# Kernel optimization log

Hardware: AMD Instinct MI355X
Metric: run time of the kernel (lower is better)

## Reference

```python
import jax, jax.numpy as jnp
import numpy as np

NUM_HEADS = 16


def setup_inputs() -> dict:
    key = jax.random.key(0)
    ks = jax.random.split(key, 6)
    B, S, D = 2, 2048, 1024
    x = jax.random.normal(ks[0], (B, S, D), dtype=jnp.float32)
    # Linear weights stored as [d_in, d_out] so forward is x @ W (qkv_bias=False)
    scale = 1.0 / np.sqrt(D)
    Wq = jax.random.normal(ks[1], (D, D), dtype=jnp.float32) * scale
    Wk = jax.random.normal(ks[2], (D, D), dtype=jnp.float32) * scale
    Wv = jax.random.normal(ks[3], (D, D), dtype=jnp.float32) * scale
    Wo = jax.random.normal(ks[4], (D, D), dtype=jnp.float32) * scale
    bo = jax.random.normal(ks[5], (D,), dtype=jnp.float32) * 0.01
    return {"x": x, "Wq": Wq, "Wk": Wk, "Wv": Wv, "Wo": Wo, "bo": bo}


def reference(x, Wq, Wk, Wv, Wo, bo):
    B, S, D = x.shape
    H = NUM_HEADS
    hd = D // H

    def split_heads(t):  # [B,S,D] -> [B,H,S,hd]
        return t.reshape(B, S, H, hd).transpose(0, 2, 1, 3)

    q = split_heads(x @ Wq)
    k = split_heads(x @ Wk)
    v = split_heads(x @ Wv)

    # full score matrix [B,H,S,S]
    scores = jnp.einsum('bhsd,bhtd->bhst', q, k)
    causal = jnp.triu(jnp.ones((S, S), dtype=bool), k=1)
    scores = jnp.where(causal, -jnp.inf, scores)
    attn = jax.nn.softmax(scores * (hd ** -0.5), axis=-1)
    # dropout p=0.0 -> identity
    out = jnp.einsum('bhst,bhtd->bhsd', attn, v)
    out = out.transpose(0, 2, 1, 3).reshape(B, S, D)
    return out @ Wo + bo
```

## Files before the change

kernel.cpp:

```cpp
#include <hip/hip_runtime.h>

typedef unsigned short ushort_t;
typedef unsigned int uint_t;
typedef __attribute__((ext_vector_type(8))) short short8;
typedef __attribute__((ext_vector_type(4))) float floatx4;

#define S_LEN 2048
#define D_DIM 1024
#define H_NUM 16
#define HD 64
#define GBUF (128 * 32)

__device__ __forceinline__ float bf2f(ushort_t u) {
    union { uint_t i; float f; } c; c.i = ((uint_t)u) << 16; return c.f;
}
__device__ __forceinline__ ushort_t f2bf(float f) {
    union { float f; uint_t i; } c; c.f = f;
    uint_t r = c.i + 0x7fffu + ((c.i >> 16) & 1u);
    return (ushort_t)(r >> 16);
}

__device__ __forceinline__ void g2l16(const ushort_t* g, ushort_t* l) {
    __builtin_amdgcn_global_load_lds(
        (const __attribute__((address_space(1))) void*)g,
        (__attribute__((address_space(3))) void*)l, 16, 0, 0);
}

__global__ __launch_bounds__(256, 4) void cast_x_kernel(
        const float* __restrict__ in, ushort_t* __restrict__ out) {
    const int idx = (blockIdx.x * 256 + threadIdx.x) * 4;
    const float4 v = *(const float4*)(in + idx);
    ushort4 o;
    o.x = f2bf(v.x); o.y = f2bf(v.y); o.z = f2bf(v.z); o.w = f2bf(v.w);
    *(ushort4*)(out + idx) = o;
}

__global__ __launch_bounds__(256, 2) void transpose4_kernel(
        const float* __restrict__ W0, const float* __restrict__ W1,
        const float* __restrict__ W2, const float* __restrict__ W3,
        ushort_t* __restrict__ T0, ushort_t* __restrict__ T1,
        ushort_t* __restrict__ T2, ushort_t* __restrict__ T3) {
    const int z = blockIdx.z;
    const float* in  = (z == 0) ? W0 : (z == 1) ? W1 : (z == 2) ? W2 : W3;
    ushort_t*    out = (z == 0) ? T0 : (z == 1) ? T1 : (z == 2) ? T2 : T3;
    __shared__ __align__(16) ushort_t t[64][65];
    const int r0 = blockIdx.y * 64, c0 = blockIdx.x * 64;
    const int tr = threadIdx.x >> 4;
    const int tc = (threadIdx.x & 15) * 4;
#pragma unroll
    for (int i = 0; i < 4; ++i) {
        const int row = tr + i * 16;
        const float4 v = *(const float4*)(in + (size_t)(r0 + row) * D_DIM + c0 + tc);
        t[row][tc + 0] = f2bf(v.x); t[row][tc + 1] = f2bf(v.y);
        t[row][tc + 2] = f2bf(v.z); t[row][tc + 3] = f2bf(v.w);
    }
    __syncthreads();
#pragma unroll
    for (int i = 0; i < 4; ++i) {
        const int n = tr + i * 16;
        ushort4 v;
        v.x = t[tc + 0][n]; v.y = t[tc + 1][n];
        v.z = t[tc + 2][n]; v.w = t[tc + 3][n];
        *(ushort4*)(out + (size_t)(c0 + n) * D_DIM + r0 + tc) = v;
    }
}

__device__ __forceinline__ void gemm_tile(
        const ushort_t* __restrict__ A, const ushort_t* __restrict__ BT,
        const int m0, const int n0,
        ushort_t* As, ushort_t* Bs, floatx4 acc[4][4]) {
    const int tid  = threadIdx.x;
    const int w    = tid >> 6;
    const int wm   = (w >> 1) * 64;
    const int wn   = (w & 1) * 64;
    const int lrow = tid & 15;
    const int kq   = ((tid & 63) >> 4) * 8;

    const int flat0 = tid * 8;
    const int flat1 = (256 + tid) * 8;
    const int row0 = flat0 >> 5, kk0 = flat0 & 31;
    const int row1 = flat1 >> 5, kk1 = flat1 & 31;

    const ushort_t* ga0 = A  + (size_t)(m0 + row0) * D_DIM + kk0;
    const ushort_t* gb0 = BT + (size_t)(n0 + row0) * D_DIM + kk0;
    const ushort_t* ga1 = A  + (size_t)(m0 + row1) * D_DIM + kk1;
    const ushort_t* gb1 = BT + (size_t)(n0 + row1) * D_DIM + kk1;

    const int nsteps = D_DIM / 32;

    g2l16(ga0, As + flat0);
    g2l16(gb0, Bs + flat0);
    g2l16(ga1, As + flat1);
    g2l16(gb1, Bs + flat1);
    g2l16(ga0 + 32, As + GBUF + flat0);
    g2l16(gb0 + 32, Bs + GBUF + flat0);
    g2l16(ga1 + 32, As + GBUF + flat1);
    g2l16(gb1 + 32, Bs + GBUF + flat1);

    int cur = 0;
    for (int k = 0; k < nsteps; ++k) {
        if (k == nsteps - 1)
            asm volatile("s_waitcnt vmcnt(0) lgkmcnt(0)" ::: "memory");
        else
            asm volatile("s_waitcnt vmcnt(4) lgkmcnt(0)" ::: "memory");
        __builtin_amdgcn_sched_barrier(0);
        __builtin_amdgcn_s_barrier();

        const ushort_t* Ac = As + cur * GBUF;
        const ushort_t* Bc = Bs + cur * GBUF;
        short8 av[4], bv[4];
#pragma unroll
        for (int i = 0; i < 4; ++i)
            av[i] = *(const short8*)(Ac + (wm + i * 16 + lrow) * 32 + kq);
#pragma unroll
        for (int j = 0; j < 4; ++j)
            bv[j] = *(const short8*)(Bc + (wn + j * 16 + lrow) * 32 + kq);

        if (k + 2 < nsteps) {
            const int nb = (cur + 2 >= 3) ? cur - 1 : cur + 2;
            ushort_t* An = As + nb * GBUF;
            ushort_t* Bn = Bs + nb * GBUF;
            const int ko = (k + 2) * 32;
            g2l16(ga0 + ko, An + flat0);
            g2l16(gb0 + ko, Bn + flat0);
            g2l16(ga1 + ko, An + flat1);
            g2l16(gb1 + ko, Bn + flat1);
        }

#pragma unroll
        for (int i = 0; i < 4; ++i)
#pragma unroll
            for (int j = 0; j < 4; ++j)
                acc[i][j] = __builtin_amdgcn_mfma_f32_16x16x32_bf16(
                    av[i], bv[j], acc[i][j], 0, 0, 0);

        cur = (cur + 1 >= 3) ? 0 : cur + 1;
    }
}

__global__ __launch_bounds__(256, 3) void gemm_qkv_kernel(
        const ushort_t* __restrict__ A,
        const ushort_t* __restrict__ WqT, const ushort_t* __restrict__ WkT,
        const ushort_t* __restrict__ WvT,
        ushort_t* __restrict__ Qo, ushort_t* __restrict__ Ko,
        ushort_t* __restrict__ Vo) {
    const ushort_t* BT = (blockIdx.z == 0) ? WqT : (blockIdx.z == 1) ? WkT : WvT;
    ushort_t* C        = (blockIdx.z == 0) ? Qo  : (blockIdx.z == 1) ? Ko  : Vo;
    const float sc     = (blockIdx.z == 0) ? 0.18033688f : 1.0f;
    __shared__ __align__(16) ushort_t As[3 * GBUF];
    __shared__ __align__(16) ushort_t Bs[3 * GBUF];
    const int m0 = blockIdx.y * 128, n0 = blockIdx.x * 128;

    floatx4 acc[4][4] = {};
    gemm_tile(A, BT, m0, n0, As, Bs, acc);

    const int tid = threadIdx.x;
    const int w = tid >> 6, wm = (w >> 1) * 64, wn = (w & 1) * 64;
    const int lrow = tid & 15;
    const int rquad = ((tid & 63) >> 4) * 4;
#pragma unroll
    for (int i = 0; i < 4; ++i) {
        const int mbase = m0 + wm + i * 16 + rquad;
#pragma unroll
        for (int j = 0; j < 4; ++j) {
            const int gn = n0 + wn + j * 16 + lrow;
#pragma unroll
            for (int r = 0; r < 4; ++r)
                C[(size_t)(mbase + r) * D_DIM + gn] = f2bf(acc[i][j][r] * sc);
        }
    }
}

__global__ __launch_bounds__(256, 2) void gemm_out_kernel(
        const ushort_t* __restrict__ A, const ushort_t* __restrict__ WoT,
        const float* __restrict__ bias, float* __restrict__ C) {
    __shared__ __align__(16) ushort_t As[3 * GBUF];
    __shared__ __align__(16) ushort_t Bs[3 * GBUF];
    const int m0 = blockIdx.y * 128, n0 = blockIdx.x * 128;

    floatx4 acc[4][4] = {};
    gemm_tile(A, WoT, m0, n0, As, Bs, acc);

    const int tid = threadIdx.x;
    const int w = tid >> 6, wm = (w >> 1) * 64, wn = (w & 1) * 64;
    const int lrow = tid & 15;
    const int rquad = ((tid & 63) >> 4) * 4;
#pragma unroll
    for (int i = 0; i < 4; ++i) {
        const int mbase = m0 + wm + i * 16 + rquad;
#pragma unroll
        for (int j = 0; j < 4; ++j) {
            const int gn = n0 + wn + j * 16 + lrow;
            const float badd = bias[gn];
#pragma unroll
            for (int r = 0; r < 4; ++r)
                C[(size_t)(mbase + r) * D_DIM + gn] = acc[i][j][r] + badd;
        }
    }
}

__global__ __launch_bounds__(256, 4) void attn_mfma_kernel(
        const ushort_t* __restrict__ Q, const ushort_t* __restrict__ K,
        const ushort_t* __restrict__ V, ushort_t* __restrict__ O) {
    __shared__ __align__(16) ushort_t Ks[64 * 64];
    __shared__ __align__(16) ushort_t Vt[64 * 64];
    __shared__ __align__(16) ushort_t Ps[4][16 * 64];

    const int bh  = blockIdx.x;
    const int b   = bh >> 4, h = bh & 15;
    const int g   = blockIdx.y & 7;
    const int p   = blockIdx.y >> 3;
    const int qt  = (p == 0) ? g : (p == 1) ? (15 - g)
                  : (p == 2) ? (16 + g) : (31 - g);
    const int q0  = qt * 64;
    const int tid = threadIdx.x;
    const int wq  = tid >> 6;
    const int lane = tid & 63;
    const int col  = lane & 15;
    const int quad = lane >> 4;
    const int c7 = col & 7;
    const int qw0  = q0 + wq * 16;
    const size_t rowbase = (size_t)b * S_LEN;
    const int ch0 = h * HD;

    const int skey = tid >> 2;
    const int schk = tid & 3;
    const int vkp = tid & 31;
    const int vdc = tid >> 5;

    short8 aq[2];
#pragma unroll
    for (int kc = 0; kc < 2; ++kc)
        aq[kc] = *(const short8*)(Q + (rowbase + qw0 + col) * D_DIM
                                    + ch0 + kc * 32 + quad * 8);

    floatx4 oacc[4] = {};
    float mrun[4], lrun[4];
#pragma unroll
    for (int r = 0; r < 4; ++r) { mrun[r] = -1e30f; lrun[r] = 0.0f; }

    const int ntiles = qt + 1;

    short8 krA, krB, vrA, vrB;
    {
        const ushort_t* kg = K + (rowbase + skey) * D_DIM + ch0 + schk * 16;
        krA = *(const short8*)(kg);
        krB = *(const short8*)(kg + 8);
        const ushort_t* vg = V + (rowbase + 2 * vkp) * D_DIM + ch0 + vdc * 8;
        vrA = *(const short8*)(vg);
        vrB = *(const short8*)(vg + D_DIM);
    }

    for (int t = 0; t < ntiles; ++t) {
        const int kb = t * 64;
        __syncthreads();
        {
            const int sw = skey & 7;
            *(short8*)(Ks + skey * 64 + (((2 * schk) ^ sw) << 3)) = krA;
            *(short8*)(Ks + skey * 64 + (((2 * schk + 1) ^ sw) << 3)) = krB;
        }
#pragma unroll
        for (int e = 0; e < 8; ++e) {
            const int d = vdc * 8 + e;
            const uint_t pk = (uint_t)(ushort_t)vrA[e] | ((uint_t)(ushort_t)vrB[e] << 16);
            *(uint_t*)(Vt + d * 64 + ((2 * vkp) ^ ((d & 7) << 3))) = pk;
        }
        {
            const int kbn = (t + 1 < ntiles) ? (t + 1) * 64 : 0;
            const ushort_t* kg = K + (rowbase + kbn + skey) * D_DIM + ch0 + schk * 16;
            krA = *(const short8*)(kg);
            krB = *(const short8*)(kg + 8);
            const ushort_t* vg = V + (rowbase + kbn + 2 * vkp) * D_DIM + ch0 + vdc * 8;
            vrA = *(const short8*)(vg);
            vrB = *(const short8*)(vg + D_DIM);
        }
        __syncthreads();

        if (kb <= qw0 + 15) {
            floatx4 sa[4] = {};
            __builtin_amdgcn_s_setprio(1);
#pragma unroll
            for (int kc = 0; kc < 2; ++kc)
#pragma unroll
                for (int j = 0; j < 4; ++j) {
                    const short8 bk = *(const short8*)(
                        Ks + (j * 16 + col) * 64 + (((kc * 4 + quad) ^ c7) << 3));
                    sa[j] = __builtin_amdgcn_mfma_f32_16x16x32_bf16(
                        aq[kc], bk, sa[j], 0, 0, 0);
                }
            __builtin_amdgcn_s_setprio(0);

            const bool needmask = (kb + 63 > qw0);
            if (needmask) {
#pragma unroll
                for (int j = 0; j < 4; ++j)
#pragma unroll
                    for (int r = 0; r < 4; ++r) {
                        const int row = qw0 + quad * 4 + r;
                        const int key = kb + j * 16 + col;
                        if (key > row) sa[j][r] = -1e30f;
                    }
            }
#pragma unroll
            for (int r = 0; r < 4; ++r) {
                float mx = fmaxf(fmaxf(sa[0][r], sa[1][r]),
                                 fmaxf(sa[2][r], sa[3][r]));
                mx = fmaxf(mx, __shfl_xor(mx, 1));
                mx = fmaxf(mx, __shfl_xor(mx, 2));
                mx = fmaxf(mx, __shfl_xor(mx, 4));
                mx = fmaxf(mx, __shfl_xor(mx, 8));
                const float mn = fmaxf(mrun[r], mx);
                const float al = __builtin_amdgcn_exp2f(mrun[r] - mn);
                mrun[r] = mn;
                float rs = 0.0f;
#pragma unroll
                for (int j = 0; j < 4; ++j) {
                    const float p2 = __builtin_amdgcn_exp2f(sa[j][r] - mn);
                    sa[j][r] = p2;
                    rs += p2;
                }
                lrun[r] = lrun[r] * al + rs;
#pragma unroll
                for (int jd = 0; jd < 4; ++jd) oacc[jd][r] *= al;
            }
            {
                ushort_t* pw = Ps[wq];
#pragma unroll
                for (int j = 0; j < 4; ++j)
#pragma unroll
                    for (int r = 0; r < 4; ++r) {
                        const int row = quad * 4 + r;
                        pw[row * 64 + ((j * 16 + col) ^ ((row & 7) << 3))] =
                            f2bf(sa[j][r]);
                    }
            }
            asm volatile("s_waitcnt lgkmcnt(0)" ::: "memory");
            __builtin_amdgcn_s_setprio(1);
#pragma unroll
            for (int kc = 0; kc < 2; ++kc) {
                const short8 ap = *(const short8*)(
                    Ps[wq] + col * 64 + (((kc * 4 + quad) ^ c7) << 3));
#pragma unroll
                for (int jd = 0; jd < 4; ++jd) {
                    const short8 bv = *(const short8*)(
                        Vt + (jd * 16 + col) * 64 + (((kc * 4 + quad) ^ c7) << 3));
                    oacc[jd] = __builtin_amdgcn_mfma_f32_16x16x32_bf16(
                        ap, bv, oacc[jd], 0, 0, 0);
                }
            }
            __builtin_amdgcn_s_setprio(0);
        }
    }

#pragma unroll
    for (int r = 0; r < 4; ++r) {
        float l = lrun[r];
        l += __shfl_xor(l, 1);
        l += __shfl_xor(l, 2);
        l += __shfl_xor(l, 4);
        l += __shfl_xor(l, 8);
        const int row = qw0 + quad * 4 + r;
        const float inv = 1.0f / l;
#pragma unroll
        for (int jd = 0; jd < 4; ++jd)
            O[(rowbase + row) * D_DIM + ch0 + jd * 16 + col] =
                f2bf(oacc[jd][r] * inv);
    }
}

extern "C" void kernel_launch(void* const* d_in, const int* in_sizes, int n_in,
                              void* d_out, int out_size, void* d_ws, size_t ws_size,
                              hipStream_t stream) {
    const float* x  = (const float*)d_in[0];
    const float* Wq = (const float*)d_in[1];
    const float* Wk = (const float*)d_in[2];
    const float* Wv = (const float*)d_in[3];
    const float* Wo = (const float*)d_in[4];
    const float* bo = (const float*)d_in[5];
    float* out = (float*)d_out;

    char* ws = (char*)d_ws;
    const size_t MB = 1024 * 1024;
    ushort_t* xb  = (ushort_t*)(ws + 0 * MB);
    ushort_t* WqT = (ushort_t*)(ws + 8 * MB);
    ushort_t* WkT = (ushort_t*)(ws + 10 * MB);
    ushort_t* WvT = (ushort_t*)(ws + 12 * MB);
    ushort_t* WoT = (ushort_t*)(ws + 14 * MB);
    ushort_t* Qb  = (ushort_t*)(ws + 16 * MB);
    ushort_t* Kb  = (ushort_t*)(ws + 24 * MB);
    ushort_t* Vb  = (ushort_t*)(ws + 32 * MB);
    ushort_t* Ob  = (ushort_t*)(ws + 40 * MB);

    cast_x_kernel<<<4096, 256, 0, stream>>>(x, xb);
    transpose4_kernel<<<dim3(16, 16, 4), 256, 0, stream>>>(
        Wq, Wk, Wv, Wo, WqT, WkT, WvT, WoT);

    gemm_qkv_kernel<<<dim3(8, 32, 3), 256, 0, stream>>>(
        xb, WqT, WkT, WvT, Qb, Kb, Vb);

    attn_mfma_kernel<<<dim3(32, 32), 256, 0, stream>>>(Qb, Kb, Vb, Ob);

    gemm_out_kernel<<<dim3(8, 32), 256, 0, stream>>>(Ob, WoT, bo, out);
}
```

Measured before the change: 194.8 us.

## Compute S transposed and pass P to PV MFMA via register permutes

Swaps the MFMA operands so each lane holds scores for one query row, which turns the row max and sum into two cross-lane shuffles instead of four per row. The probabilities are packed with the hardware bf16 convert and rearranged into the A-operand layout with ds_bpermute, so the per-wave shared-memory P buffer and its wait are gone. The rescale factors and final normalizer are broadcast back to the output layout with bpermute. This trades LDS stores and loads for more permute instructions and extra register pressure.

```diff
diff --git a/kernel.cpp b/kernel.cpp
--- a/kernel.cpp
+++ b/kernel.cpp
@@ -18,6 +18,11 @@
     union { float f; uint_t i; } c; c.f = f;
     uint_t r = c.i + 0x7fffu + ((c.i >> 16) & 1u);
     return (ushort_t)(r >> 16);
+}
+__device__ __forceinline__ uint_t cvtpk_bf16(float lo, float hi) {
+    uint_t d;
+    asm("v_cvt_pk_bf16_f32 %0, %1, %2" : "=v"(d) : "v"(lo), "v"(hi));
+    return d;
 }
 
 __device__ __forceinline__ void g2l16(const ushort_t* g, ushort_t* l) {
@@ -204,7 +209,6 @@
         const ushort_t* __restrict__ V, ushort_t* __restrict__ O) {
     __shared__ __align__(16) ushort_t Ks[64 * 64];
     __shared__ __align__(16) ushort_t Vt[64 * 64];
-    __shared__ __align__(16) ushort_t Ps[4][16 * 64];
 
     const int bh  = blockIdx.x;
     const int b   = bh >> 4, h = bh & 15;
@@ -222,6 +226,8 @@
     const int qw0  = q0 + wq * 16;
     const size_t rowbase = (size_t)b * S_LEN;
     const int ch0 = h * HD;
+    const int q4 = quad * 4;
+    const int gbase = (lane & 48) << 2;
 
     const int skey = tid >> 2;
     const int schk = tid & 3;
@@ -235,9 +241,7 @@
                                     + ch0 + kc * 32 + quad * 8);
 
     floatx4 oacc[4] = {};
-    float mrun[4], lrun[4];
-#pragma unroll
-    for (int r = 0; r < 4; ++r) { mrun[r] = -1e30f; lrun[r] = 0.0f; }
+    float mrun0 = -1e30f, lrun0 = 0.0f;
 
     const int ntiles = qt + 1;
 
@@ -262,8 +266,8 @@
 #pragma unroll
         for (int e = 0; e < 8; ++e) {
             const int d = vdc * 8 + e;
-            const uint_t pk = (uint_t)(ushort_t)vrA[e] | ((uint_t)(ushort_t)vrB[e] << 16);
-            *(uint_t*)(Vt + d * 64 + ((2 * vkp) ^ ((d & 7) << 3))) = pk;
+            const uint_t pkv = (uint_t)(ushort_t)vrA[e] | ((uint_t)(ushort_t)vrB[e] << 16);
+            *(uint_t*)(Vt + d * 64 + ((2 * vkp) ^ ((d & 7) << 3))) = pkv;
         }
         {
             const int kbn = (t + 1 < ntiles) ? (t + 1) * 64 : 0;
@@ -286,81 +290,95 @@
                     const short8 bk = *(const short8*)(
                         Ks + (j * 16 + col) * 64 + (((kc * 4 + quad) ^ c7) << 3));
                     sa[j] = __builtin_amdgcn_mfma_f32_16x16x32_bf16(
-                        aq[kc], bk, sa[j], 0, 0, 0);
+                        bk, aq[kc], sa[j], 0, 0, 0);
                 }
             __builtin_amdgcn_s_setprio(0);
 
             const bool needmask = (kb + 63 > qw0);
             if (needmask) {
+                const int qrow = qw0 + col;
 #pragma unroll
                 for (int j = 0; j < 4; ++j)
 #pragma unroll
-                    for (int r = 0; r < 4; ++r) {
-                        const int row = qw0 + quad * 4 + r;
-                        const int key = kb + j * 16 + col;
-                        if (key > row) sa[j][r] = -1e30f;
-                    }
+                    for (int r = 0; r < 4; ++r)
+                        if (kb + j * 16 + q4 + r > qrow) sa[j][r] = -1e30f;
             }
-#pragma unroll
-            for (int r = 0; r < 4; ++r) {
-                float mx = fmaxf(fmaxf(sa[0][r], sa[1][r]),
-                                 fmaxf(sa[2][r], sa[3][r]));
-                mx = fmaxf(mx, __shfl_xor(mx, 1));
-                mx = fmaxf(mx, __shfl_xor(mx, 2));
-                mx = fmaxf(mx, __shfl_xor(mx, 4));
-                mx = fmaxf(mx, __shfl_xor(mx, 8));
-                const float mn = fmaxf(mrun[r], mx);
-                const float al = __builtin_amdgcn_exp2f(mrun[r] - mn);
-                mrun[r] = mn;
-                float rs = 0.0f;
-#pragma unroll
-                for (int j = 0; j < 4; ++j) {
+            float mx = sa[0][0];
+#pragma unroll
+            for (int j = 0; j < 4; ++j)
+#pragma unroll
+                for (int r = 0; r < 4; ++r) mx = fmaxf(mx, sa[j][r]);
+            mx = fmaxf(mx, __shfl_xor(mx, 16));
+            mx = fmaxf(mx, __shfl_xor(mx, 32));
+            const float mn = fmaxf(mrun0, mx);
+            const float al = __builtin_amdgcn_exp2f(mrun0 - mn);
+            mrun0 = mn;
+            float rs = 0.0f;
+#pragma unroll
+            for (int j = 0; j < 4; ++j)
+#pragma unroll
+                for (int r = 0; r < 4; ++r) {
                     const float p2 = __builtin_amdgcn_exp2f(sa[j][r] - mn);
                     sa[j][r] = p2;
                     rs += p2;
                 }
-                lrun[r] = lrun[r] * al + rs;
-#pragma unroll
-                for (int jd = 0; jd < 4; ++jd) oacc[jd][r] *= al;
+            lrun0 = lrun0 * al + rs;
+            float al4[4];
+#pragma unroll
+            for (int r = 0; r < 4; ++r)
+                al4[r] = __int_as_float(__builtin_amdgcn_ds_bpermute(
+                    gbase + ((q4 + r) << 2), __float_as_int(al)));
+#pragma unroll
+            for (int jd = 0; jd < 4; ++jd)
+#pragma unroll
+                for (int r = 0; r < 4; ++r) oacc[jd][r] *= al4[r];
+            uint_t pk[4][2];
+#pragma unroll
+            for (int j = 0; j < 4; ++j) {
+                pk[j][0] = cvtpk_bf16(sa[j][0], sa[j][1]);
+                pk[j][1] = cvtpk_bf16(sa[j][2], sa[j][3]);
             }
-            {
-                ushort_t* pw = Ps[wq];
-#pragma unroll
-                for (int j = 0; j < 4; ++j)
-#pragma unroll
-                    for (int r = 0; r < 4; ++r) {
-                        const int row = quad * 4 + r;
-                        pw[row * 64 + ((j * 16 + col) ^ ((row & 7) << 3))] =
-                            f2bf(sa[j][r]);
-                    }
-            }
-            asm volatile("s_waitcnt lgkmcnt(0)" ::: "memory");
+            const int aLo = (col + ((quad & 1) << 5)) << 2;
+            const int aHi = aLo + 64;
+            uint_t res[4][2][2];
+#pragma unroll
+            for (int j = 0; j < 4; ++j)
+#pragma unroll
+                for (int p2 = 0; p2 < 2; ++p2) {
+                    res[j][p2][0] = (uint_t)__builtin_amdgcn_ds_bpermute(aLo, (int)pk[j][p2]);
+                    res[j][p2][1] = (uint_t)__builtin_amdgcn_ds_bpermute(aHi, (int)pk[j][p2]);
+                }
+            const bool b5 = (quad >> 1) != 0;
+            union { short8 s; uint_t u[4]; } ap[2];
+#pragma unroll
+            for (int kc = 0; kc < 2; ++kc)
+#pragma unroll
+                for (int d = 0; d < 4; ++d)
+                    ap[kc].u[d] = b5 ? res[2 * kc + 1][d & 1][d >> 1]
+                                     : res[2 * kc][d & 1][d >> 1];
             __builtin_amdgcn_s_setprio(1);
 #pragma unroll
-            for (int kc = 0; kc < 2; ++kc) {
-                const short8 ap = *(const short8*)(
-                    Ps[wq] + col * 64 + (((kc * 4 + quad) ^ c7) << 3));
+            for (int kc = 0; kc < 2; ++kc)
 #pragma unroll
                 for (int jd = 0; jd < 4; ++jd) {
                     const short8 bv = *(const short8*)(
                         Vt + (jd * 16 + col) * 64 + (((kc * 4 + quad) ^ c7) << 3));
                     oacc[jd] = __builtin_amdgcn_mfma_f32_16x16x32_bf16(
-                        ap, bv, oacc[jd], 0, 0, 0);
+                        ap[kc].s, bv, oacc[jd], 0, 0, 0);
                 }
-            }
             __builtin_amdgcn_s_setprio(0);
         }
     }
 
+    float l = lrun0;
+    l += __shfl_xor(l, 16);
+    l += __shfl_xor(l, 32);
 #pragma unroll
     for (int r = 0; r < 4; ++r) {
-        float l = lrun[r];
-        l += __shfl_xor(l, 1);
-        l += __shfl_xor(l, 2);
-        l += __shfl_xor(l, 4);
-        l += __shfl_xor(l, 8);
-        const int row = qw0 + quad * 4 + r;
-        const float inv = 1.0f / l;
+        const float lr = __int_as_float(__builtin_amdgcn_ds_bpermute(
+            gbase + ((q4 + r) << 2), __float_as_int(l)));
+        const float inv = 1.0f / lr;
+        const int row = qw0 + q4 + r;
 #pragma unroll
         for (int jd = 0; jd < 4; ++jd)
             O[(rowbase + row) * D_DIM + ch0 + jd * 16 + col] =
```

Measured after the change: 187.9 us, median of 2. -3.5%, faster.
